# Kernel tuning notes

Hardware: AMD Instinct MI355X
Metric: run time of the kernel (lower is better)

The kernel has to match this reference:

```python
import jax, jax.numpy as jnp
import numpy as np
from jax import lax

BN_EPS = 1e-3  # keras BatchNormalization default epsilon
DN = ('NHWC', 'HWIO', 'NHWC')


def ste_sign(x):
    # larq ste_sign forward: sign with sign(0) -> +1
    return jnp.where(x >= 0, 1.0, -1.0).astype(x.dtype)


def bn_inference(x, beta, mean, var):
    # scale=False -> no gamma, center=True -> beta
    return (x - mean) * lax.rsqrt(var + BN_EPS) + beta


def setup_inputs() -> dict:
    key = jax.random.key(0)
    ks = jax.random.split(key, 8)
    C = 256
    x = jax.random.normal(ks[0], (32, 56, 56, C), dtype=jnp.float32)
    w1 = jax.random.normal(ks[1], (3, 3, C, C), dtype=jnp.float32) * 0.05
    w2 = jax.random.normal(ks[2], (3, 3, C, C), dtype=jnp.float32) * 0.05
    beta1 = jax.random.normal(ks[3], (C,), dtype=jnp.float32) * 0.1
    beta2 = jax.random.normal(ks[4], (C,), dtype=jnp.float32) * 0.1
    mean1 = jax.random.normal(ks[5], (C,), dtype=jnp.float32) * 0.1
    mean2 = jax.random.normal(ks[6], (C,), dtype=jnp.float32) * 0.1
    var1 = jax.random.uniform(ks[7], (C,), dtype=jnp.float32, minval=0.5, maxval=1.5)
    var2 = jax.random.uniform(jax.random.fold_in(key, 7), (C,), dtype=jnp.float32, minval=0.5, maxval=1.5)
    return {"x": x, "w1": w1, "beta1": beta1, "mean1": mean1, "var1": var1,
            "w2": w2, "beta2": beta2, "mean2": mean2, "var2": var2}


def reference(x, w1, beta1, mean1, var1, w2, beta2, mean2, var2):
    # conv_1: quantized input and quantized weights (XNOR conv), stride 1, SAME
    h = lax.conv_general_dilated(ste_sign(x), ste_sign(w1), (1, 1), 'SAME',
                                 dimension_numbers=DN)
    h = bn_inference(h, beta1, mean1, var1)
    # conv_2: quantized input and weights
    h = lax.conv_general_dilated(ste_sign(h), ste_sign(w2), (1, 1), 'SAME',
                                 dimension_numbers=DN)
    # max pool 2x2 stride 2
    h = lax.reduce_window(h, -jnp.inf, lax.max, (1, 2, 2, 1), (1, 2, 2, 1), 'VALID')
    h = bn_inference(h, beta2, mean2, var2)
    return h
```

## Files before the change

kernel.cpp:

```cpp
#include <hip/hip_runtime.h>
#include <stdint.h>

#define BN_EPS 1e-3f

constexpr int Bn = 32, H = 56, Wd = 56, C = 256;
constexpr int NSLOT = 232;
typedef int v4i __attribute__((ext_vector_type(4)));

__device__ __forceinline__ int imax(int a, int b) { return a > b ? a : b; }

__global__ __launch_bounds__(256) void k_sign_x(const float* __restrict__ x,
                                                int8_t* __restrict__ xs, int n4) {
  int i = blockIdx.x * 256 + threadIdx.x;
  if (i >= n4) return;
  float4 v = ((const float4*)x)[i];
  char4 s;
  s.x = v.x >= 0.f ? 1 : -1;
  s.y = v.y >= 0.f ? 1 : -1;
  s.z = v.z >= 0.f ? 1 : -1;
  s.w = v.w >= 0.f ? 1 : -1;
  ((char4*)xs)[i] = s;
}

__global__ __launch_bounds__(256) void k_sign_wT2(const float* __restrict__ w,
                                                  uint32_t* __restrict__ wt) {
  int u = blockIdx.x * 256 + threadIdx.x;
  int f = u >> 8, r = u & 255;
  int l = r >> 2, w4 = r & 3;
  int grp = l >> 4, lid = l & 15;
  int tap = f >> 6, icq = (f >> 4) & 3, ocg = f & 15;
  int oc = ocg * 16 + lid;
  uint32_t pk = 0;
#pragma unroll
  for (int j = 0; j < 4; ++j) {
    int ic = icq * 64 + grp * 16 + w4 * 4 + j;
    float v = w[((size_t)(tap * 256 + ic)) * 256 + oc];
    pk |= (v >= 0.f ? 0x01u : 0xFFu) << (8 * j);
  }
  wt[u] = pk;
}

template <int MODE>
__device__ __forceinline__ void conv_body(
    const int8_t* As, const int8_t* __restrict__ wT2, int wn, int lane,
    const float* __restrict__ beta, const float* __restrict__ mean,
    const float* __restrict__ var, int8_t* __restrict__ hs,
    float* __restrict__ outp, int b, int rp)
{
  const int grp = lane >> 4, lid = lane & 15;
  const int wbase = wn * 32;
  const int cstg = grp << 4;

  int sb[7];
#pragma unroll
  for (int ms = 0; ms < 7; ++ms) {
    const int m = ms * 16 + lid;
    sb[ms] = (m & 1) * 58 + (m >> 1);
  }

  const int8_t* bpl = wT2 + (size_t)wn * 2048 + (size_t)lane * 16;

  v4i acc[7][2];
#pragma unroll
  for (int i = 0; i < 7; ++i)
#pragma unroll
    for (int j = 0; j < 2; ++j) acc[i][j] = (v4i){0, 0, 0, 0};

#define LOADB(dst, st)                                                     \
  {                                                                        \
    const int8_t* p_ = bpl + (size_t)(st) * 16384;                         \
    dst[0] = *(const v4i*)(p_);                                            \
    dst[1] = *(const v4i*)(p_ + 1024);                                     \
  }

#define LOADA(dst, st)                                                     \
  {                                                                        \
    const int tap_ = (st) >> 2, icq_ = (st) & 3;                           \
    const int ky_ = (tap_ >= 6) ? 2 : ((tap_ >= 3) ? 1 : 0);               \
    const int kx_ = tap_ - 3 * ky_;                                        \
    const int D_ = ky_ * 58 + kx_;                                         \
    const int ko_ = cstg + icq_ * 64;                                      \
    _Pragma("unroll") for (int ms = 0; ms < 7; ++ms) {                     \
      const int s_ = sb[ms] + D_;                                          \
      dst[ms] = *(const v4i*)(As + (s_ << 8) + (ko_ ^ ((s_ & 7) << 4)));   \
    }                                                                      \
  }

#define MFMAC(af, bf)                                                      \
  __builtin_amdgcn_s_setprio(1);                                           \
  _Pragma("unroll") for (int ms = 0; ms < 7; ++ms)                         \
  _Pragma("unroll") for (int ns = 0; ns < 2; ++ns)                         \
      acc[ms][ns] = __builtin_amdgcn_mfma_i32_16x16x64_i8(                 \
          af[ms], bf[ns], acc[ms][ns], 0, 0, 0);                           \
  __builtin_amdgcn_s_setprio(0);

  v4i af[7], bfA[2], bfB[2];
  LOADB(bfA, 0)

#pragma unroll 1
  for (int i = 0; i < 18; ++i) {
    const int s0 = 2 * i, s1 = 2 * i + 1;
    const int s2 = (s1 + 1 > 35) ? 35 : s1 + 1;
    LOADB(bfB, s1)
    LOADA(af, s0)
    MFMAC(af, bfA)
    LOADB(bfA, s2)
    LOADA(af, s1)
    MFMAC(af, bfB)
  }

#undef MFMAC
#undef LOADA
#undef LOADB

  const int rA = rp * 2;
  if (MODE == 0) {
#pragma unroll
    for (int ns = 0; ns < 2; ++ns) {
      const int oc = wbase + ns * 16 + lid;
      const float mu = mean[oc], rs = rsqrtf(var[oc] + BN_EPS), be = beta[oc];
#pragma unroll
      for (int ms = 0; ms < 7; ++ms)
#pragma unroll
        for (int q = 0; q < 4; ++q) {
          const int m = ms * 16 + grp * 4 + q;
          const int lr = m & 1, col = m >> 1;
          const float bnv = ((float)acc[ms][ns][q] - mu) * rs + be;
          hs[(((size_t)(b * 56 + rA + lr)) * 56 + col) * 256 + oc] =
              bnv >= 0.f ? (int8_t)1 : (int8_t)-1;
        }
    }
  } else {
#pragma unroll
    for (int ns = 0; ns < 2; ++ns) {
      const int oc = wbase + ns * 16 + lid;
      const float mu = mean[oc], rs = rsqrtf(var[oc] + BN_EPS), be = beta[oc];
#pragma unroll
      for (int ms = 0; ms < 7; ++ms) {
        const int mx = imax(imax(acc[ms][ns][0], acc[ms][ns][1]),
                            imax(acc[ms][ns][2], acc[ms][ns][3]));
        const int j = ms * 4 + grp;
        outp[(((size_t)(b * 28 + rp)) * 28 + j) * 256 + oc] =
            ((float)mx - mu) * rs + be;
      }
    }
  }
}

template <int MODE>
__global__ __launch_bounds__(512, 4) void k_conv(
    const int8_t* __restrict__ src, const int8_t* __restrict__ wT2,
    const float* __restrict__ beta, const float* __restrict__ mean,
    const float* __restrict__ var,
    int8_t* __restrict__ hs, float* __restrict__ outp)
{
  const int t = threadIdx.x;
  const int rp = blockIdx.x;
  const int b = blockIdx.y;
  const int rr0 = rp * 2;

  __shared__ __align__(16) int8_t As[NSLOT * 256];

  for (int i = t; i < NSLOT * 16; i += 512) {
    const int s = i >> 4, c = i & 15;
    const int lr = s / 58, colst = s - lr * 58;
    const int sr = rr0 + lr - 1, sc = colst - 1;
    uint4 v;
    v.x = v.y = v.z = v.w = 0u;
    if ((unsigned)sr < 56u && (unsigned)sc < 56u)
      v = *(const uint4*)(src + (((size_t)(b * 56 + sr)) * 56 + sc) * 256 + c * 16);
    *(uint4*)(As + (s << 8) + ((c << 4) ^ ((s & 7) << 4))) = v;
  }
  __syncthreads();

  const int lane = t & 63;
  const int wn = t >> 6;
  conv_body<MODE>(As, wT2, wn, lane, beta, mean, var, hs, outp, b, rp);
}

extern "C" void kernel_launch(void* const* d_in, const int* in_sizes, int n_in,
                              void* d_out, int out_size, void* d_ws, size_t ws_size,
                              hipStream_t stream) {
  const float* x     = (const float*)d_in[0];
  const float* w1    = (const float*)d_in[1];
  const float* beta1 = (const float*)d_in[2];
  const float* mean1 = (const float*)d_in[3];
  const float* var1  = (const float*)d_in[4];
  const float* w2    = (const float*)d_in[5];
  const float* beta2 = (const float*)d_in[6];
  const float* mean2 = (const float*)d_in[7];
  const float* var2  = (const float*)d_in[8];
  float* out = (float*)d_out;

  const size_t NPIX = (size_t)Bn * H * Wd * C;
  int8_t* xs  = (int8_t*)d_ws;
  int8_t* hs  = xs + NPIX;
  int8_t* w1t = hs + NPIX;
  int8_t* w2t = w1t + 589824;

  k_sign_x<<<dim3((int)(NPIX / 4 / 256)), 256, 0, stream>>>(x, xs, (int)(NPIX / 4));
  k_sign_wT2<<<dim3(576), 256, 0, stream>>>(w1, (uint32_t*)w1t);
  k_sign_wT2<<<dim3(576), 256, 0, stream>>>(w2, (uint32_t*)w2t);
  k_conv<0><<<dim3(28, Bn), 512, 0, stream>>>(xs, w1t, beta1, mean1, var1, hs, nullptr);
  k_conv<1><<<dim3(28, Bn), 512, 0, stream>>>(hs, w2t, beta2, mean2, var2, nullptr, out);
}
```

Before: 136.0 us.

## Replace XOR-swizzled LDS layout with padded stride and fully unroll K loop

The shared-memory tile changes from an XOR-swizzled 256-byte row layout to a padded 272-byte row stride. With the padding, every A-fragment address becomes a per-lane base pointer plus a compile-time constant, so the 36-step K loop is fully unrolled with immediate LDS offsets and double-buffered B loads. This is meant to remove per-iteration address arithmetic and keep LDS bank conflicts low through padding instead of swizzling. In exchange, LDS use grows slightly and the fully unrolled loop adds code size and register pressure under launch_bounds(512,4).

```diff
diff --git a/kernel.cpp b/kernel.cpp
--- a/kernel.cpp
+++ b/kernel.cpp
@@ -5,6 +5,7 @@
 
 constexpr int Bn = 32, H = 56, Wd = 56, C = 256;
 constexpr int NSLOT = 232;
+constexpr int SSTRIDE = 272;
 typedef int v4i __attribute__((ext_vector_type(4)));
 
 __device__ __forceinline__ int imax(int a, int b) { return a > b ? a : b; }
@@ -40,6 +41,12 @@
   wt[u] = pk;
 }
 
+__device__ constexpr int aoff(int s) {
+  const int tap = s >> 2, icq = s & 3;
+  const int ky = tap / 3, kx = tap - 3 * ky;
+  return (ky * 58 + kx) * SSTRIDE + icq * 64;
+}
+
 template <int MODE>
 __device__ __forceinline__ void conv_body(
     const int8_t* As, const int8_t* __restrict__ wT2, int wn, int lane,
@@ -49,16 +56,16 @@
 {
   const int grp = lane >> 4, lid = lane & 15;
   const int wbase = wn * 32;
-  const int cstg = grp << 4;
 
-  int sb[7];
+  const int8_t* qb[7];
 #pragma unroll
   for (int ms = 0; ms < 7; ++ms) {
     const int m = ms * 16 + lid;
-    sb[ms] = (m & 1) * 58 + (m >> 1);
+    const int sb = (m & 1) * 58 + (m >> 1);
+    qb[ms] = As + sb * SSTRIDE + (grp << 4);
   }
 
-  const int8_t* bpl = wT2 + (size_t)wn * 2048 + (size_t)lane * 16;
+  const int8_t* bq = wT2 + (size_t)wn * 2048 + (size_t)lane * 16;
 
   v4i acc[7][2];
 #pragma unroll
@@ -66,52 +73,32 @@
 #pragma unroll
     for (int j = 0; j < 2; ++j) acc[i][j] = (v4i){0, 0, 0, 0};
 
-#define LOADB(dst, st)                                                     \
-  {                                                                        \
-    const int8_t* p_ = bpl + (size_t)(st) * 16384;                         \
-    dst[0] = *(const v4i*)(p_);                                            \
-    dst[1] = *(const v4i*)(p_ + 1024);                                     \
+  v4i bf[2][2];
+  bf[0][0] = *(const v4i*)(bq);
+  bf[0][1] = *(const v4i*)(bq + 1024);
+  bq += 16384;
+
+#pragma unroll
+  for (int s = 0; s < 36; ++s) {
+    const int pb = s & 1;
+    if (s + 1 < 36) {
+      bf[pb ^ 1][0] = *(const v4i*)(bq);
+      bf[pb ^ 1][1] = *(const v4i*)(bq + 1024);
+      bq += 16384;
+    }
+    v4i af[7];
+#pragma unroll
+    for (int ms = 0; ms < 7; ++ms)
+      af[ms] = *(const v4i*)(qb[ms] + aoff(s));
+    __builtin_amdgcn_s_setprio(1);
+#pragma unroll
+    for (int ms = 0; ms < 7; ++ms)
+#pragma unroll
+      for (int ns = 0; ns < 2; ++ns)
+        acc[ms][ns] = __builtin_amdgcn_mfma_i32_16x16x64_i8(
+            af[ms], bf[pb][ns], acc[ms][ns], 0, 0, 0);
+    __builtin_amdgcn_s_setprio(0);
   }
-
-#define LOADA(dst, st)                                                     \
-  {                                                                        \
-    const int tap_ = (st) >> 2, icq_ = (st) & 3;                           \
-    const int ky_ = (tap_ >= 6) ? 2 : ((tap_ >= 3) ? 1 : 0);               \
-    const int kx_ = tap_ - 3 * ky_;                                        \
-    const int D_ = ky_ * 58 + kx_;                                         \
-    const int ko_ = cstg + icq_ * 64;                                      \
-    _Pragma("unroll") for (int ms = 0; ms < 7; ++ms) {                     \
-      const int s_ = sb[ms] + D_;                                          \
-      dst[ms] = *(const v4i*)(As + (s_ << 8) + (ko_ ^ ((s_ & 7) << 4)));   \
-    }                                                                      \
-  }
-
-#define MFMAC(af, bf)                                                      \
-  __builtin_amdgcn_s_setprio(1);                                           \
-  _Pragma("unroll") for (int ms = 0; ms < 7; ++ms)                         \
-  _Pragma("unroll") for (int ns = 0; ns < 2; ++ns)                         \
-      acc[ms][ns] = __builtin_amdgcn_mfma_i32_16x16x64_i8(                 \
-          af[ms], bf[ns], acc[ms][ns], 0, 0, 0);                           \
-  __builtin_amdgcn_s_setprio(0);
-
-  v4i af[7], bfA[2], bfB[2];
-  LOADB(bfA, 0)
-
-#pragma unroll 1
-  for (int i = 0; i < 18; ++i) {
-    const int s0 = 2 * i, s1 = 2 * i + 1;
-    const int s2 = (s1 + 1 > 35) ? 35 : s1 + 1;
-    LOADB(bfB, s1)
-    LOADA(af, s0)
-    MFMAC(af, bfA)
-    LOADB(bfA, s2)
-    LOADA(af, s1)
-    MFMAC(af, bfB)
-  }
-
-#undef MFMAC
-#undef LOADA
-#undef LOADB
 
   const int rA = rp * 2;
   if (MODE == 0) {
@@ -159,7 +146,7 @@
   const int b = blockIdx.y;
   const int rr0 = rp * 2;
 
-  __shared__ __align__(16) int8_t As[NSLOT * 256];
+  __shared__ __align__(16) int8_t As[NSLOT * SSTRIDE];
 
   for (int i = t; i < NSLOT * 16; i += 512) {
     const int s = i >> 4, c = i & 15;
@@ -169,7 +156,7 @@
     v.x = v.y = v.z = v.w = 0u;
     if ((unsigned)sr < 56u && (unsigned)sc < 56u)
       v = *(const uint4*)(src + (((size_t)(b * 56 + sr)) * 56 + sc) * 256 + c * 16);
-    *(uint4*)(As + (s << 8) + ((c << 4) ^ ((s & 7) << 4))) = v;
+    *(uint4*)(As + s * SSTRIDE + c * 16) = v;
   }
   __syncthreads();
 
```

Measured after the change: 136.2 us. No clear change (+0.2%).

## Enlarge conv block tile to four output rows with 16 waves

Applied to the files above, without the earlier changes.

Each conv block now processes four output rows (two pooled rows) using 1024 threads arranged as 2 M-waves by 8 N-waves, with a larger shared-memory halo tile. This lowers the halo overhead per output and lets each weight fragment loaded from global memory serve more pixels. In exchange it halves the grid size and uses larger blocks, which may hurt occupancy and load balance across CUs.

```diff
diff --git a/kernel.cpp b/kernel.cpp
--- a/kernel.cpp
+++ b/kernel.cpp
@@ -4,7 +4,7 @@
 #define BN_EPS 1e-3f
 
 constexpr int Bn = 32, H = 56, Wd = 56, C = 256;
-constexpr int NSLOT = 232;
+constexpr int NSLOT = 348;
 typedef int v4i __attribute__((ext_vector_type(4)));
 
 __device__ __forceinline__ int imax(int a, int b) { return a > b ? a : b; }
@@ -40,22 +40,32 @@
   wt[u] = pk;
 }
 
+__device__ __forceinline__ void mdecode(int mm, int& row, int& col) {
+  const int qd = mm >> 2, q = mm & 3;
+  const int p = (qd >= 28) ? 1 : 0;
+  const int j = qd - 28 * p;
+  col = 2 * j + (q & 1);
+  row = 2 * p + (q >> 1);
+}
+
 template <int MODE>
 __device__ __forceinline__ void conv_body(
-    const int8_t* As, const int8_t* __restrict__ wT2, int wn, int lane,
+    const int8_t* As, const int8_t* __restrict__ wT2, int wm, int wn, int lane,
     const float* __restrict__ beta, const float* __restrict__ mean,
     const float* __restrict__ var, int8_t* __restrict__ hs,
     float* __restrict__ outp, int b, int rp)
 {
   const int grp = lane >> 4, lid = lane & 15;
+  const int MSB = wm * 7;
   const int wbase = wn * 32;
   const int cstg = grp << 4;
 
   int sb[7];
 #pragma unroll
   for (int ms = 0; ms < 7; ++ms) {
-    const int m = ms * 16 + lid;
-    sb[ms] = (m & 1) * 58 + (m >> 1);
+    int row, col;
+    mdecode((MSB + ms) * 16 + lid, row, col);
+    sb[ms] = row * 58 + col;
   }
 
   const int8_t* bpl = wT2 + (size_t)wn * 2048 + (size_t)lane * 16;
@@ -113,7 +123,7 @@
 #undef LOADA
 #undef LOADB
 
-  const int rA = rp * 2;
+  const int rA = rp * 4;
   if (MODE == 0) {
 #pragma unroll
     for (int ns = 0; ns < 2; ++ns) {
@@ -123,10 +133,10 @@
       for (int ms = 0; ms < 7; ++ms)
 #pragma unroll
         for (int q = 0; q < 4; ++q) {
-          const int m = ms * 16 + grp * 4 + q;
-          const int lr = m & 1, col = m >> 1;
+          int row, col;
+          mdecode((MSB + ms) * 16 + grp * 4 + q, row, col);
           const float bnv = ((float)acc[ms][ns][q] - mu) * rs + be;
-          hs[(((size_t)(b * 56 + rA + lr)) * 56 + col) * 256 + oc] =
+          hs[(((size_t)(b * 56 + rA + row)) * 56 + col) * 256 + oc] =
               bnv >= 0.f ? (int8_t)1 : (int8_t)-1;
         }
     }
@@ -139,8 +149,10 @@
       for (int ms = 0; ms < 7; ++ms) {
         const int mx = imax(imax(acc[ms][ns][0], acc[ms][ns][1]),
                             imax(acc[ms][ns][2], acc[ms][ns][3]));
-        const int j = ms * 4 + grp;
-        outp[(((size_t)(b * 28 + rp)) * 28 + j) * 256 + oc] =
+        const int qd = (MSB + ms) * 4 + grp;
+        const int p = (qd >= 28) ? 1 : 0;
+        const int j = qd - 28 * p;
+        outp[(((size_t)(b * 28 + rp * 2 + p)) * 28 + j) * 256 + oc] =
             ((float)mx - mu) * rs + be;
       }
     }
@@ -148,7 +160,7 @@
 }
 
 template <int MODE>
-__global__ __launch_bounds__(512, 4) void k_conv(
+__global__ __launch_bounds__(1024, 4) void k_conv(
     const int8_t* __restrict__ src, const int8_t* __restrict__ wT2,
     const float* __restrict__ beta, const float* __restrict__ mean,
     const float* __restrict__ var,
@@ -157,11 +169,11 @@
   const int t = threadIdx.x;
   const int rp = blockIdx.x;
   const int b = blockIdx.y;
-  const int rr0 = rp * 2;
+  const int rr0 = rp * 4;
 
   __shared__ __align__(16) int8_t As[NSLOT * 256];
 
-  for (int i = t; i < NSLOT * 16; i += 512) {
+  for (int i = t; i < NSLOT * 16; i += 1024) {
     const int s = i >> 4, c = i & 15;
     const int lr = s / 58, colst = s - lr * 58;
     const int sr = rr0 + lr - 1, sc = colst - 1;
@@ -174,8 +186,9 @@
   __syncthreads();
 
   const int lane = t & 63;
-  const int wn = t >> 6;
-  conv_body<MODE>(As, wT2, wn, lane, beta, mean, var, hs, outp, b, rp);
+  const int wv = t >> 6;
+  const int wm = wv >> 3, wn = wv & 7;
+  conv_body<MODE>(As, wT2, wm, wn, lane, beta, mean, var, hs, outp, b, rp);
 }
 
 extern "C" void kernel_launch(void* const* d_in, const int* in_sizes, int n_in,
@@ -201,6 +214,6 @@
   k_sign_x<<<dim3((int)(NPIX / 4 / 256)), 256, 0, stream>>>(x, xs, (int)(NPIX / 4));
   k_sign_wT2<<<dim3(576), 256, 0, stream>>>(w1, (uint32_t*)w1t);
   k_sign_wT2<<<dim3(576), 256, 0, stream>>>(w2, (uint32_t*)w2t);
-  k_conv<0><<<dim3(28, Bn), 512, 0, stream>>>(xs, w1t, beta1, mean1, var1, hs, nullptr);
-  k_conv<1><<<dim3(28, Bn), 512, 0, stream>>>(hs, w2t, beta2, mean2, var2, nullptr, out);
-}
+  k_conv<0><<<dim3(14, Bn), 1024, 0, stream>>>(xs, w1t, beta1, mean1, var1, hs, nullptr);
+  k_conv<1><<<dim3(14, Bn), 1024, 0, stream>>>(hs, w2t, beta2, mean2, var2, nullptr, out);
+}
```

Result: slower. 144.7 us (+6.5%).
